# Kernel tuning notes

Measured on AMD Instinct MI355X. Metric: run time of the kernel, lower is better.

## Reference

```python
import jax, jax.numpy as jnp
import numpy as np

K = 3
DILATION = 1
DG = 1  # deformable groups


def _deform_conv2d(x, offsets, mask, weight, bias, k=K, dilation=DILATION, dg=DG):
    # x: [B, C, H, W]; offsets: [B, dg*2*k*k, H, W]; mask: [B, dg*k*k, H, W]
    # weight: [O, C, k, k]; bias: [O]
    B, C, H, W = x.shape
    O = weight.shape[0]
    Cg = C // dg
    kk = k * k
    pad = (k // 2) * dilation

    # base sampling grid per kernel tap (stride=1)
    ky, kx = jnp.meshgrid(jnp.arange(k), jnp.arange(k), indexing='ij')
    ky = ky.reshape(kk)
    kx = kx.reshape(kk)
    base_y = (jnp.arange(H)[None, :, None] - pad + ky[:, None, None] * dilation)  # [kk,H,1]
    base_x = (jnp.arange(W)[None, None, :] - pad + kx[:, None, None] * dilation)  # [kk,1,W]

    off = offsets.reshape(B, dg, kk, 2, H, W)
    py = base_y[None, None].astype(x.dtype) + off[:, :, :, 0]  # [B,dg,kk,H,W]
    px = base_x[None, None].astype(x.dtype) + off[:, :, :, 1]  # [B,dg,kk,H,W]

    y0 = jnp.floor(py)
    x0 = jnp.floor(px)
    wy1 = py - y0  # frac weights
    wx1 = px - x0
    wy0 = 1.0 - wy1
    wx0 = 1.0 - wx1

    img = x.reshape(B, dg, Cg, H * W)

    def gather(yi, xi):
        # yi, xi: float integer-valued coords [B,dg,kk,H,W]; zero outside bounds
        valid = (yi >= 0) & (yi <= H - 1) & (xi >= 0) & (xi <= W - 1)
        yc = jnp.clip(yi, 0, H - 1).astype(jnp.int32)
        xc = jnp.clip(xi, 0, W - 1).astype(jnp.int32)
        idx = (yc * W + xc).reshape(B, dg, 1, kk * H * W)
        vals = jnp.take_along_axis(img, idx, axis=3).reshape(B, dg, Cg, kk, H, W)
        return vals * valid.reshape(B, dg, 1, kk, H, W).astype(x.dtype)

    def w5(a):  # lift [B,dg,kk,H,W] -> [B,dg,1,kk,H,W]
        return a.reshape(B, dg, 1, kk, H, W)

    sampled = (gather(y0, x0) * w5(wy0 * wx0)
               + gather(y0, x0 + 1) * w5(wy0 * wx1)
               + gather(y0 + 1, x0) * w5(wy1 * wx0)
               + gather(y0 + 1, x0 + 1) * w5(wy1 * wx1))  # [B,dg,Cg,kk,H,W]

    sampled = sampled * mask.reshape(B, dg, 1, kk, H, W)
    sampled = sampled.reshape(B, C, kk, H, W)

    out = jnp.einsum('bckhw,ock->bohw', sampled, weight.reshape(O, C, kk))
    return out + bias[None, :, None, None]


def setup_inputs() -> dict:
    key = jax.random.key(0)
    k1, k2, k3, k4, k5 = jax.random.split(key, 5)
    B, C, O, H, W = 8, 128, 128, 64, 64
    x = jax.random.normal(k1, (B, C, H, W), dtype=jnp.float32)
    offsets = jax.random.normal(k2, (B, DG * 2 * K * K, H, W), dtype=jnp.float32)
    mask = jax.random.uniform(k3, (B, DG * K * K, H, W), dtype=jnp.float32)
    fan_in = C * K * K
    weight = jax.random.normal(k4, (O, C, K, K), dtype=jnp.float32) / np.sqrt(fan_in)
    bias = jax.random.normal(k5, (O,), dtype=jnp.float32) * 0.01
    return {"x": x, "offsets": offsets, "mask": mask, "weight": weight, "bias": bias}


def reference(x, offsets, mask, weight, bias):
    return _deform_conv2d(x, offsets, mask, weight, bias)
```

## Files before the change

### kernel.cpp

```cpp
#include <hip/hip_runtime.h>
#include <math.h>

constexpr int Bn = 8, Cn = 128, On = 128, Hn = 64, Wn = 64;
constexpr int KK = 9, PAD = 1, BDIM = 256;
constexpr int CG = 16;
constexpr int NG = Cn / CG;
constexpr int KG = 160;
constexpr int KTOT = NG * KG;
constexpr int BANDH = 10;
constexpr int XST = 656;
constexpr int AST = 168;
constexpr int ME = KK * Wn;

typedef __attribute__((ext_vector_type(8))) short bf16x8;
typedef __attribute__((ext_vector_type(4))) float f32x4;
typedef unsigned short u16;
typedef unsigned int u32;

__device__ inline u16 f2bf(float f) {
    union { float f; u32 u; } v; v.f = f;
    return (u16)((v.u + 0x7FFFu + ((v.u >> 16) & 1u)) >> 16);
}

__global__ void wprep_kernel(const float* __restrict__ w, u16* __restrict__ wbf) {
    const int e = blockIdx.x * BDIM + threadIdx.x;
    const int o  = e / KTOT;
    const int kp = e - o * KTOT;
    const int g  = kp / KG;
    const int r  = kp - g * KG;
    const int t  = r >> 4;
    const int cl = r & 15;
    float v = 0.f;
    if (t < KK) v = w[o * (Cn * KK) + (g * CG + cl) * KK + t];
    wbf[e] = f2bf(v);
}

__global__ __launch_bounds__(BDIM, 2)
void dcn_mfma_kernel(const float* __restrict__ x,
                     const float* __restrict__ offs,
                     const float* __restrict__ mask,
                     const u16*   __restrict__ wbf,
                     const float* __restrict__ bias,
                     float* __restrict__ out)
{
    __shared__ float xband[CG * XST];
    __shared__ u16   ash[Wn * AST];

    const int tid = threadIdx.x;
    const int b   = blockIdx.x & 7;
    const int h   = blockIdx.x >> 3;
    const int r0  = min(max(h - 4, 0), Hn - BANDH);

    const int cl16 = tid >> 4, l16b = tid & 15;
    float4 bnd[BANDH];
    {
        const float* xp = x + (((size_t)(b * Cn + cl16)) << 12) + r0 * Wn + (l16b << 2);
        #pragma unroll
        for (int r = 0; r < BANDH; ++r) bnd[r] = *(const float4*)(xp + r * Wn);
    }

    float4 mw[3]; int2 mq[3]; int2 mi[3];
    #pragma unroll
    for (int it = 0; it < 3; ++it) {
        mw[it] = make_float4(0.f, 0.f, 0.f, 0.f);
        mq[it] = make_int2(r0 << 8, r0 << 8);
        mi[it] = make_int2(7, 7);
        const int e = tid + it * BDIM;
        if (e < ME) {
            const int t = e >> 6, px = e & 63;
            const int ty = t / 3, tx = t - ty * 3;
            const float oy = offs[((b * 18 + 2 * t    ) * Hn + h) * Wn + px];
            const float ox = offs[((b * 18 + 2 * t + 1) * Hn + h) * Wn + px];
            const float m  = mask[((b * KK + t) * Hn + h) * Wn + px];
            const float py = (float)(h - PAD + ty) + oy;
            const float qx = (float)(px - PAD + tx) + ox;
            const float fy = floorf(py), fx = floorf(qx);
            const float wy1 = py - fy, wx1 = qx - fx;
            const float wy0 = 1.f - wy1, wx0 = 1.f - wx1;
            const int y0 = (int)fy, x0 = (int)fx;
            const bool cx0 = (x0 >= 0) && (x0 < Wn);
            const bool cx1 = (x0 >= -1) && (x0 < Wn - 1);
            const float wr[2] = { wy0, wy1 };
            float wout[4]; int qout[2], iout[2];
            #pragma unroll
            for (int j = 0; j < 2; ++j) {
                const int yr = y0 + j;
                const bool rv = (yr >= 0) && (yr < Hn);
                wout[2 * j]     = (rv && cx0) ? wr[j] * wx0 * m : 0.f;
                wout[2 * j + 1] = (rv && cx1) ? wr[j] * wx1 * m : 0.f;
                int qv;
                if (!rv || (!cx0 && !cx1)) qv = r0 << 8;
                else                       qv = (yr << 8) | (x0 + 1);
                const bool inband = (qv >> 8) >= r0 && (qv >> 8) < r0 + BANDH;
                qout[j] = inband ? qv : ~qv;
                iout[j] = (((qv >> 8) - r0) << 6) + (qv & 255) + 7;
            }
            mw[it] = make_float4(wout[0], wout[1], wout[2], wout[3]);
            mq[it] = make_int2(qout[0], qout[1]);
            mi[it] = make_int2(iout[0], iout[1]);
        }
    }

    {
        float* dp = &xband[cl16 * XST + 8 + (l16b << 2)];
        #pragma unroll
        for (int r = 0; r < BANDH; ++r) *(float4*)(dp + r * 64) = bnd[r];
        const int padi = (l16b < 8) ? l16b : (640 + l16b);
        xband[cl16 * XST + padi] = 0.f;
        const int px = tid & 63, kz = 144 + ((tid >> 6) << 2);
        u16* d = &ash[px * AST + kz];
        d[0] = 0; d[1] = 0; d[2] = 0; d[3] = 0;
    }
    __syncthreads();

    const int wv = tid >> 6, ln = tid & 63, quad = ln >> 4, l16 = ln & 15;
    const u16* wrow0 = wbf + (size_t)(wv * 32 + l16) * KTOT;

    f32x4 acc[2][4];
    #pragma unroll
    for (int mt = 0; mt < 2; ++mt)
        #pragma unroll
        for (int nt = 0; nt < 4; ++nt) acc[mt][nt] = (f32x4){0.f, 0.f, 0.f, 0.f};

    for (int g = 0; g < NG; ++g) {
        #pragma unroll
        for (int it = 0; it < 3; ++it) {
            const int e = tid + it * BDIM;
            if (e < ME) {
                const int t = e >> 6, px = e & 63;
                const float4 w  = mw[it];
                const int2   q  = mq[it];
                const int2   ix = mi[it];
                u16 av[CG];
                if (!__any((q.x | q.y) < 0)) {
                    #pragma unroll
                    for (int cl = 0; cl < CG; ++cl) {
                        const float* xc = &xband[cl * XST];
                        const float t0 = xc[ix.x], t1 = xc[ix.x + 1];
                        const float b0 = xc[ix.y], b1 = xc[ix.y + 1];
                        av[cl] = f2bf(fmaf(w.x, t0, fmaf(w.y, t1,
                                      fmaf(w.z, b0, w.w * b1))));
                    }
                } else {
                    const int qx = q.x < 0 ? ~q.x : q.x;
                    const int qy = q.y < 0 ? ~q.y : q.y;
                    const int yrx = qx >> 8, yry = qy >> 8;
                    const int xx = (qx & 255) - 1, xy = (qy & 255) - 1;
                    const int ax0 = max(xx, 0), ax1 = min(xx + 1, Wn - 1);
                    const int ay0 = max(xy, 0), ay1 = min(xy + 1, Wn - 1);
                    const float* gp = x + (((size_t)(b * Cn + g * CG)) << 12);
                    for (int cl = 0; cl < CG; ++cl) {
                        const float* gc = gp + (cl << 12);
                        const float t0 = gc[yrx * Wn + ax0], t1 = gc[yrx * Wn + ax1];
                        const float b0 = gc[yry * Wn + ay0], b1 = gc[yry * Wn + ay1];
                        av[cl] = f2bf(fmaf(w.x, t0, fmaf(w.y, t1,
                                      fmaf(w.z, b0, w.w * b1))));
                    }
                }
                u32 pk[8];
                #pragma unroll
                for (int q2 = 0; q2 < 8; ++q2)
                    pk[q2] = (u32)av[2 * q2] | ((u32)av[2 * q2 + 1] << 16);
                u32* d = (u32*)&ash[px * AST + (t << 4)];
                *(uint4*)d       = make_uint4(pk[0], pk[1], pk[2], pk[3]);
                *(uint4*)(d + 4) = make_uint4(pk[4], pk[5], pk[6], pk[7]);
            }
        }
        __syncthreads();

        if (g + 1 < NG) {
            const float* xp = x + (((size_t)(b * Cn + (g + 1) * CG + cl16)) << 12)
                              + r0 * Wn + (l16b << 2);
            #pragma unroll
            for (int r = 0; r < BANDH; ++r) bnd[r] = *(const float4*)(xp + r * Wn);
        }

        #pragma unroll
        for (int s = 0; s < 5; ++s) {
            const int kg = g * KG + s * 32 + quad * 8;
            const int kl = s * 32 + quad * 8;
            const bf16x8 a0 = *(const bf16x8*)(wrow0 + kg);
            const bf16x8 a1 = *(const bf16x8*)(wrow0 + 16 * KTOT + kg);
            const bf16x8 b0 = *(const bf16x8*)&ash[(0 * 16 + l16) * AST + kl];
            const bf16x8 b1 = *(const bf16x8*)&ash[(1 * 16 + l16) * AST + kl];
            const bf16x8 b2 = *(const bf16x8*)&ash[(2 * 16 + l16) * AST + kl];
            const bf16x8 b3 = *(const bf16x8*)&ash[(3 * 16 + l16) * AST + kl];
            acc[0][0] = __builtin_amdgcn_mfma_f32_16x16x32_bf16(a0, b0, acc[0][0], 0, 0, 0);
            acc[0][1] = __builtin_amdgcn_mfma_f32_16x16x32_bf16(a0, b1, acc[0][1], 0, 0, 0);
            acc[0][2] = __builtin_amdgcn_mfma_f32_16x16x32_bf16(a0, b2, acc[0][2], 0, 0, 0);
            acc[0][3] = __builtin_amdgcn_mfma_f32_16x16x32_bf16(a0, b3, acc[0][3], 0, 0, 0);
            acc[1][0] = __builtin_amdgcn_mfma_f32_16x16x32_bf16(a1, b0, acc[1][0], 0, 0, 0);
            acc[1][1] = __builtin_amdgcn_mfma_f32_16x16x32_bf16(a1, b1, acc[1][1], 0, 0, 0);
            acc[1][2] = __builtin_amdgcn_mfma_f32_16x16x32_bf16(a1, b2, acc[1][2], 0, 0, 0);
            acc[1][3] = __builtin_amdgcn_mfma_f32_16x16x32_bf16(a1, b3, acc[1][3], 0, 0, 0);
        }

        if (g + 1 < NG) {
            float* dp = &xband[cl16 * XST + 8 + (l16b << 2)];
            #pragma unroll
            for (int r = 0; r < BANDH; ++r) *(float4*)(dp + r * 64) = bnd[r];
        }
        __syncthreads();
    }

    float* ob = out + (((size_t)b * On) * Hn + h) * Wn;
    #pragma unroll
    for (int mt = 0; mt < 2; ++mt)
        #pragma unroll
        for (int nt = 0; nt < 4; ++nt)
            #pragma unroll
            for (int r = 0; r < 4; ++r) {
                const int o  = wv * 32 + mt * 16 + quad * 4 + r;
                const int px = nt * 16 + l16;
                ob[(size_t)o * (Hn * Wn) + px] = acc[mt][nt][r] + bias[o];
            }
}

constexpr int FB_PXB = 32, FB_CCH = 4, FB_NCT = FB_CCH * KK, FB_MW = KK * FB_PXB;

#define FMA4(A, S, W)                          \
    A.x = fmaf((S).x, (W), A.x);               \
    A.y = fmaf((S).y, (W), A.y);               \
    A.z = fmaf((S).z, (W), A.z);               \
    A.w = fmaf((S).w, (W), A.w);

__global__ __launch_bounds__(BDIM, 4)
void dcn_fb_kernel(const float* __restrict__ x,
                   const float* __restrict__ offs,
                   const float* __restrict__ mask,
                   const float* __restrict__ weight,
                   const float* __restrict__ bias,
                   float* __restrict__ out)
{
    __shared__ float wmeta[4 * FB_MW];
    __shared__ int   imeta[4 * FB_MW];
    __shared__ float ssh[FB_NCT * FB_PXB];
    __shared__ float wsh[FB_NCT * On];

    const int tid    = threadIdx.x;
    const int b      = blockIdx.x & 7;
    const int rem    = blockIdx.x >> 3;
    const int h      = rem >> 1;
    const int pxbase = (rem & 1) * FB_PXB;

    for (int e = tid; e < FB_MW; e += BDIM) {
        const int t  = e >> 5;
        const int px = e & 31;
        const int pg = pxbase + px;
        const int ty = t / 3, tx = t - ty * 3;
        const float oy = offs[((b * 18 + 2 * t    ) * Hn + h) * Wn + pg];
        const float ox = offs[((b * 18 + 2 * t + 1) * Hn + h) * Wn + pg];
        const float m  = mask[((b * KK + t) * Hn + h) * Wn + pg];
        const float py = (float)(h - PAD + ty) + oy;
        const float qx = (float)(pg - PAD + tx) + ox;
        const float y0 = floorf(py), x0 = floorf(qx);
        const float wy1 = py - y0, wx1 = qx - x0;
        const float wy0 = 1.f - wy1, wx0 = 1.f - wx1;
        const float cw[4] = { wy0 * wx0, wy0 * wx1, wy1 * wx0, wy1 * wx1 };
        #pragma unroll
        for (int k = 0; k < 4; ++k) {
            const float yk = y0 + (float)(k >> 1);
            const float xk = x0 + (float)(k & 1);
            const bool valid = (yk >= 0.f) && (yk <= (float)(Hn - 1)) &&
                               (xk >= 0.f) && (xk <= (float)(Wn - 1));
            const int yc = (int)fminf(fmaxf(yk, 0.f), (float)(Hn - 1));
            const int xc = (int)fminf(fmaxf(xk, 0.f), (float)(Wn - 1));
            wmeta[k * FB_MW + e] = valid ? cw[k] * m : 0.f;
            imeta[k * FB_MW + e] = yc * Wn + xc;
        }
    }
    __syncthreads();

    const int px0 = (tid & 7) << 2;
    const int oo  = (tid >> 3) << 2;

    float4 acc[4];
    #pragma unroll
    for (int j = 0; j < 4; ++j) acc[j] = make_float4(0.f, 0.f, 0.f, 0.f);

    for (int cb = 0; cb < Cn / FB_CCH; ++cb) {
        #pragma unroll
        for (int it = 0; it < (FB_NCT * On) / BDIM; ++it) {
            const int e = tid + it * BDIM;
            const int r = e >> 7;
            const int o = e & 127;
            wsh[r * On + o] = weight[o * (Cn * KK) + cb * FB_NCT + r];
        }
        for (int e = tid; e < FB_NCT * FB_PXB; e += BDIM) {
            const int px = e & 31;
            const int ct = e >> 5;
            const int c  = ct / 9;
            const int mb = (ct - c * 9) * FB_PXB + px;
            const float* xp = x + (((b * Cn) + cb * FB_CCH + c) << 12);
            float v =  wmeta[mb]              * xp[imeta[mb]];
            v = fmaf(wmeta[FB_MW     + mb], xp[imeta[FB_MW     + mb]], v);
            v = fmaf(wmeta[2 * FB_MW + mb], xp[imeta[2 * FB_MW + mb]], v);
            v = fmaf(wmeta[3 * FB_MW + mb], xp[imeta[3 * FB_MW + mb]], v);
            ssh[ct * FB_PXB + px] = v;
        }
        __syncthreads();

        #pragma unroll 6
        for (int ct = 0; ct < FB_NCT; ++ct) {
            const float4 sv = *(const float4*)&ssh[ct * FB_PXB + px0];
            const float4 wa = *(const float4*)&wsh[ct * On + oo];
            FMA4(acc[0], sv, wa.x);
            FMA4(acc[1], sv, wa.y);
            FMA4(acc[2], sv, wa.z);
            FMA4(acc[3], sv, wa.w);
        }
        __syncthreads();
    }

    #pragma unroll
    for (int j = 0; j < 4; ++j) {
        const float bv = bias[oo + j];
        float4 r = acc[j];
        r.x += bv; r.y += bv; r.z += bv; r.w += bv;
        *(float4*)&out[((b * On + oo + j) * Hn + h) * Wn + pxbase + px0] = r;
    }
}

extern "C" void kernel_launch(void* const* d_in, const int* in_sizes, int n_in,
                              void* d_out, int out_size, void* d_ws, size_t ws_size,
                              hipStream_t stream) {
    const float* x      = (const float*)d_in[0];
    const float* offs   = (const float*)d_in[1];
    const float* mask   = (const float*)d_in[2];
    const float* weight = (const float*)d_in[3];
    const float* bias   = (const float*)d_in[4];
    float* out = (float*)d_out;

    const size_t need = (size_t)On * KTOT * sizeof(u16);
    if (d_ws != nullptr && ws_size >= need) {
        u16* wbf = (u16*)d_ws;
        wprep_kernel<<<dim3(On * KTOT / BDIM), dim3(BDIM), 0, stream>>>(weight, wbf);
        dcn_mfma_kernel<<<dim3(Bn * Hn), dim3(BDIM), 0, stream>>>(
            x, offs, mask, wbf, bias, out);
    } else {
        dcn_fb_kernel<<<dim3(Bn * Hn * 2), dim3(BDIM), 0, stream>>>(
            x, offs, mask, weight, bias, out);
    }
}
```

Baseline: 157.5 us.

## Split MFMA deform-conv blocks into half-row tiles with bf16 channel-pair band

Each block now handles 32 output pixels instead of 64, doubling the grid and raising launch bounds to 4 blocks per CU to improve occupancy. The input band is stored in shared memory as bf16 channel pairs, which halves LDS footprint and the number of LDS reads per bilinear sample. Shared-memory strides are padded to odd word counts to avoid bank conflicts. Output is staged through LDS for coalesced float4 stores. The trade-off is extra rounding of the input to bf16 before interpolation, and the weight rows are reloaded by twice as many blocks.

```diff
diff --git a/kernel.cpp b/kernel.cpp
--- a/kernel.cpp
+++ b/kernel.cpp
@@ -3,14 +3,15 @@
 
 constexpr int Bn = 8, Cn = 128, On = 128, Hn = 64, Wn = 64;
 constexpr int KK = 9, PAD = 1, BDIM = 256;
+constexpr int PXB = 32;
 constexpr int CG = 16;
 constexpr int NG = Cn / CG;
 constexpr int KG = 160;
 constexpr int KTOT = NG * KG;
 constexpr int BANDH = 10;
-constexpr int XST = 656;
-constexpr int AST = 168;
-constexpr int ME = KK * Wn;
+constexpr int XSTP = 657;
+constexpr int AST = 170;
+constexpr int ME = KK * PXB;
 
 typedef __attribute__((ext_vector_type(8))) short bf16x8;
 typedef __attribute__((ext_vector_type(4))) float f32x4;
@@ -21,6 +22,11 @@
     union { float f; u32 u; } v; v.f = f;
     return (u16)((v.u + 0x7FFFu + ((v.u >> 16) & 1u)) >> 16);
 }
+__device__ inline u32 pk2bf(float a, float b) {
+    return (u32)f2bf(a) | ((u32)f2bf(b) << 16);
+}
+__device__ inline float bflo(u32 w) { return __uint_as_float(w << 16); }
+__device__ inline float bfhi(u32 w) { return __uint_as_float(w & 0xFFFF0000u); }
 
 __global__ void wprep_kernel(const float* __restrict__ w, u16* __restrict__ wbf) {
     const int e = blockIdx.x * BDIM + threadIdx.x;
@@ -35,7 +41,7 @@
     wbf[e] = f2bf(v);
 }
 
-__global__ __launch_bounds__(BDIM, 2)
+__global__ __launch_bounds__(BDIM, 4)
 void dcn_mfma_kernel(const float* __restrict__ x,
                      const float* __restrict__ offs,
                      const float* __restrict__ mask,
@@ -43,37 +49,45 @@
                      const float* __restrict__ bias,
                      float* __restrict__ out)
 {
-    __shared__ float xband[CG * XST];
-    __shared__ u16   ash[Wn * AST];
-
-    const int tid = threadIdx.x;
-    const int b   = blockIdx.x & 7;
-    const int h   = blockIdx.x >> 3;
-    const int r0  = min(max(h - 4, 0), Hn - BANDH);
-
-    const int cl16 = tid >> 4, l16b = tid & 15;
-    float4 bnd[BANDH];
+    __shared__ __align__(16) u32 pband[8 * XSTP];
+    __shared__ __align__(16) u16 ash[PXB * AST];
+
+    const int tid    = threadIdx.x;
+    const int b      = blockIdx.x & 7;
+    const int rem    = blockIdx.x >> 3;
+    const int h      = rem >> 1;
+    const int pxbase = (rem & 1) * PXB;
+    const int r0     = min(max(h - 4, 0), Hn - BANDH);
+
+    const int s_px4  = tid & 15;
+    const int s_pair = (tid >> 4) & 7;
+    float4 bnda[5], bndb[5];
     {
-        const float* xp = x + (((size_t)(b * Cn + cl16)) << 12) + r0 * Wn + (l16b << 2);
-        #pragma unroll
-        for (int r = 0; r < BANDH; ++r) bnd[r] = *(const float4*)(xp + r * Wn);
-    }
-
-    float4 mw[3]; int2 mq[3]; int2 mi[3];
-    #pragma unroll
-    for (int it = 0; it < 3; ++it) {
+        #pragma unroll
+        for (int it = 0; it < 5; ++it) {
+            const int row = (tid + it * BDIM) >> 7;
+            const float* base = x + (((size_t)(b * Cn + 2 * s_pair)) << 12)
+                                + (r0 + row) * Wn + (s_px4 << 2);
+            bnda[it] = *(const float4*)base;
+            bndb[it] = *(const float4*)(base + 4096);
+        }
+    }
+
+    float4 mw[2]; int2 mq[2]; int2 mi[2];
+    #pragma unroll
+    for (int it = 0; it < 2; ++it) {
         mw[it] = make_float4(0.f, 0.f, 0.f, 0.f);
         mq[it] = make_int2(r0 << 8, r0 << 8);
         mi[it] = make_int2(7, 7);
         const int e = tid + it * BDIM;
         if (e < ME) {
-            const int t = e >> 6, px = e & 63;
+            const int t = e >> 5, px = e & 31, pg = pxbase + px;
             const int ty = t / 3, tx = t - ty * 3;
-            const float oy = offs[((b * 18 + 2 * t    ) * Hn + h) * Wn + px];
-            const float ox = offs[((b * 18 + 2 * t + 1) * Hn + h) * Wn + px];
-            const float m  = mask[((b * KK + t) * Hn + h) * Wn + px];
+            const float oy = offs[((b * 18 + 2 * t    ) * Hn + h) * Wn + pg];
+            const float ox = offs[((b * 18 + 2 * t + 1) * Hn + h) * Wn + pg];
+            const float m  = mask[((b * KK + t) * Hn + h) * Wn + pg];
             const float py = (float)(h - PAD + ty) + oy;
-            const float qx = (float)(px - PAD + tx) + ox;
+            const float qx = (float)(pg - PAD + tx) + ox;
             const float fy = floorf(py), fx = floorf(qx);
             const float wy1 = py - fy, wx1 = qx - fx;
             const float wy0 = 1.f - wy1, wx0 = 1.f - wx1;
@@ -102,44 +116,53 @@
     }
 
     {
-        float* dp = &xband[cl16 * XST + 8 + (l16b << 2)];
-        #pragma unroll
-        for (int r = 0; r < BANDH; ++r) *(float4*)(dp + r * 64) = bnd[r];
-        const int padi = (l16b < 8) ? l16b : (640 + l16b);
-        xband[cl16 * XST + padi] = 0.f;
-        const int px = tid & 63, kz = 144 + ((tid >> 6) << 2);
-        u16* d = &ash[px * AST + kz];
-        d[0] = 0; d[1] = 0; d[2] = 0; d[3] = 0;
+        #pragma unroll
+        for (int it = 0; it < 5; ++it) {
+            const int row = (tid + it * BDIM) >> 7;
+            u32* d = &pband[s_pair * XSTP + row * 64 + 8 + (s_px4 << 2)];
+            d[0] = pk2bf(bnda[it].x, bndb[it].x);
+            d[1] = pk2bf(bnda[it].y, bndb[it].y);
+            d[2] = pk2bf(bnda[it].z, bndb[it].z);
+            d[3] = pk2bf(bnda[it].w, bndb[it].w);
+        }
+        if (tid < 128) {
+            const int pr = tid >> 4, ws = tid & 15;
+            pband[pr * XSTP + (ws < 8 ? ws : 640 + ws)] = 0;
+        }
+        ((u32*)ash)[(tid >> 3) * 85 + 72 + (tid & 7)] = 0;
     }
     __syncthreads();
 
     const int wv = tid >> 6, ln = tid & 63, quad = ln >> 4, l16 = ln & 15;
     const u16* wrow0 = wbf + (size_t)(wv * 32 + l16) * KTOT;
 
-    f32x4 acc[2][4];
+    f32x4 acc[2][2];
     #pragma unroll
     for (int mt = 0; mt < 2; ++mt)
         #pragma unroll
-        for (int nt = 0; nt < 4; ++nt) acc[mt][nt] = (f32x4){0.f, 0.f, 0.f, 0.f};
+        for (int nt = 0; nt < 2; ++nt) acc[mt][nt] = (f32x4){0.f, 0.f, 0.f, 0.f};
 
     for (int g = 0; g < NG; ++g) {
         #pragma unroll
-        for (int it = 0; it < 3; ++it) {
+        for (int it = 0; it < 2; ++it) {
             const int e = tid + it * BDIM;
             if (e < ME) {
-                const int t = e >> 6, px = e & 63;
+                const int t = e >> 5, px = e & 31;
                 const float4 w  = mw[it];
                 const int2   q  = mq[it];
                 const int2   ix = mi[it];
-                u16 av[CG];
+                u32 avp[8];
                 if (!__any((q.x | q.y) < 0)) {
                     #pragma unroll
-                    for (int cl = 0; cl < CG; ++cl) {
-                        const float* xc = &xband[cl * XST];
-                        const float t0 = xc[ix.x], t1 = xc[ix.x + 1];
-                        const float b0 = xc[ix.y], b1 = xc[ix.y + 1];
-                        av[cl] = f2bf(fmaf(w.x, t0, fmaf(w.y, t1,
-                                      fmaf(w.z, b0, w.w * b1))));
+                    for (int c2 = 0; c2 < 8; ++c2) {
+                        const u32* pc = &pband[c2 * XSTP];
+                        const u32 wt0 = pc[ix.x], wt1 = pc[ix.x + 1];
+                        const u32 wb0 = pc[ix.y], wb1 = pc[ix.y + 1];
+                        const float va = fmaf(w.x, bflo(wt0), fmaf(w.y, bflo(wt1),
+                                         fmaf(w.z, bflo(wb0), w.w * bflo(wb1))));
+                        const float vb = fmaf(w.x, bfhi(wt0), fmaf(w.y, bfhi(wt1),
+                                         fmaf(w.z, bfhi(wb0), w.w * bfhi(wb1))));
+                        avp[c2] = pk2bf(va, vb);
                     }
                 } else {
                     const int qx = q.x < 0 ? ~q.x : q.x;
@@ -149,71 +172,91 @@
                     const int ax0 = max(xx, 0), ax1 = min(xx + 1, Wn - 1);
                     const int ay0 = max(xy, 0), ay1 = min(xy + 1, Wn - 1);
                     const float* gp = x + (((size_t)(b * Cn + g * CG)) << 12);
-                    for (int cl = 0; cl < CG; ++cl) {
-                        const float* gc = gp + (cl << 12);
-                        const float t0 = gc[yrx * Wn + ax0], t1 = gc[yrx * Wn + ax1];
-                        const float b0 = gc[yry * Wn + ay0], b1 = gc[yry * Wn + ay1];
-                        av[cl] = f2bf(fmaf(w.x, t0, fmaf(w.y, t1,
-                                      fmaf(w.z, b0, w.w * b1))));
+                    for (int c2 = 0; c2 < 8; ++c2) {
+                        float v2[2];
+                        for (int sb = 0; sb < 2; ++sb) {
+                            const float* gc = gp + ((2 * c2 + sb) << 12);
+                            const float t0 = gc[yrx * Wn + ax0], t1 = gc[yrx * Wn + ax1];
+                            const float b0 = gc[yry * Wn + ay0], b1 = gc[yry * Wn + ay1];
+                            v2[sb] = fmaf(w.x, t0, fmaf(w.y, t1,
+                                     fmaf(w.z, b0, w.w * b1)));
+                        }
+                        avp[c2] = pk2bf(v2[0], v2[1]);
                     }
                 }
-                u32 pk[8];
+                u32* d = (u32*)ash + px * 85 + t * 8;
                 #pragma unroll
-                for (int q2 = 0; q2 < 8; ++q2)
-                    pk[q2] = (u32)av[2 * q2] | ((u32)av[2 * q2 + 1] << 16);
-                u32* d = (u32*)&ash[px * AST + (t << 4)];
-                *(uint4*)d       = make_uint4(pk[0], pk[1], pk[2], pk[3]);
-                *(uint4*)(d + 4) = make_uint4(pk[4], pk[5], pk[6], pk[7]);
+                for (int j = 0; j < 8; ++j) d[j] = avp[j];
             }
         }
         __syncthreads();
 
         if (g + 1 < NG) {
-            const float* xp = x + (((size_t)(b * Cn + (g + 1) * CG + cl16)) << 12)
-                              + r0 * Wn + (l16b << 2);
-            #pragma unroll
-            for (int r = 0; r < BANDH; ++r) bnd[r] = *(const float4*)(xp + r * Wn);
-        }
-
+            #pragma unroll
+            for (int it = 0; it < 5; ++it) {
+                const int row = (tid + it * BDIM) >> 7;
+                const float* base = x + (((size_t)(b * Cn + (g + 1) * CG + 2 * s_pair)) << 12)
+                                    + (r0 + row) * Wn + (s_px4 << 2);
+                bnda[it] = *(const float4*)base;
+                bndb[it] = *(const float4*)(base + 4096);
+            }
+        }
+
+        const u32* ad = (const u32*)ash;
         #pragma unroll
         for (int s = 0; s < 5; ++s) {
             const int kg = g * KG + s * 32 + quad * 8;
-            const int kl = s * 32 + quad * 8;
             const bf16x8 a0 = *(const bf16x8*)(wrow0 + kg);
             const bf16x8 a1 = *(const bf16x8*)(wrow0 + 16 * KTOT + kg);
-            const bf16x8 b0 = *(const bf16x8*)&ash[(0 * 16 + l16) * AST + kl];
-            const bf16x8 b1 = *(const bf16x8*)&ash[(1 * 16 + l16) * AST + kl];
-            const bf16x8 b2 = *(const bf16x8*)&ash[(2 * 16 + l16) * AST + kl];
-            const bf16x8 b3 = *(const bf16x8*)&ash[(3 * 16 + l16) * AST + kl];
-            acc[0][0] = __builtin_amdgcn_mfma_f32_16x16x32_bf16(a0, b0, acc[0][0], 0, 0, 0);
-            acc[0][1] = __builtin_amdgcn_mfma_f32_16x16x32_bf16(a0, b1, acc[0][1], 0, 0, 0);
-            acc[0][2] = __builtin_amdgcn_mfma_f32_16x16x32_bf16(a0, b2, acc[0][2], 0, 0, 0);
-            acc[0][3] = __builtin_amdgcn_mfma_f32_16x16x32_bf16(a0, b3, acc[0][3], 0, 0, 0);
-            acc[1][0] = __builtin_amdgcn_mfma_f32_16x16x32_bf16(a1, b0, acc[1][0], 0, 0, 0);
-            acc[1][1] = __builtin_amdgcn_mfma_f32_16x16x32_bf16(a1, b1, acc[1][1], 0, 0, 0);
-            acc[1][2] = __builtin_amdgcn_mfma_f32_16x16x32_bf16(a1, b2, acc[1][2], 0, 0, 0);
-            acc[1][3] = __builtin_amdgcn_mfma_f32_16x16x32_bf16(a1, b3, acc[1][3], 0, 0, 0);
+            union BF { bf16x8 v; u32 w[4]; } b0, b1;
+            const int kd = s * 16 + quad * 4;
+            #pragma unroll
+            for (int j = 0; j < 4; ++j) {
+                b0.w[j] = ad[(0 * 16 + l16) * 85 + kd + j];
+                b1.w[j] = ad[(1 * 16 + l16) * 85 + kd + j];
+            }
+            acc[0][0] = __builtin_amdgcn_mfma_f32_16x16x32_bf16(a0, b0.v, acc[0][0], 0, 0, 0);
+            acc[0][1] = __builtin_amdgcn_mfma_f32_16x16x32_bf16(a0, b1.v, acc[0][1], 0, 0, 0);
+            acc[1][0] = __builtin_amdgcn_mfma_f32_16x16x32_bf16(a1, b0.v, acc[1][0], 0, 0, 0);
+            acc[1][1] = __builtin_amdgcn_mfma_f32_16x16x32_bf16(a1, b1.v, acc[1][1], 0, 0, 0);
         }
 
         if (g + 1 < NG) {
-            float* dp = &xband[cl16 * XST + 8 + (l16b << 2)];
-            #pragma unroll
-            for (int r = 0; r < BANDH; ++r) *(float4*)(dp + r * 64) = bnd[r];
+            #pragma unroll
+            for (int it = 0; it < 5; ++it) {
+                const int row = (tid + it * BDIM) >> 7;
+                u32* d = &pband[s_pair * XSTP + row * 64 + 8 + (s_px4 << 2)];
+                d[0] = pk2bf(bnda[it].x, bndb[it].x);
+                d[1] = pk2bf(bnda[it].y, bndb[it].y);
+                d[2] = pk2bf(bnda[it].z, bndb[it].z);
+                d[3] = pk2bf(bnda[it].w, bndb[it].w);
+            }
         }
         __syncthreads();
     }
 
-    float* ob = out + (((size_t)b * On) * Hn + h) * Wn;
+    float* tr = (float*)pband;
     #pragma unroll
     for (int mt = 0; mt < 2; ++mt)
         #pragma unroll
-        for (int nt = 0; nt < 4; ++nt)
+        for (int nt = 0; nt < 2; ++nt)
             #pragma unroll
             for (int r = 0; r < 4; ++r) {
                 const int o  = wv * 32 + mt * 16 + quad * 4 + r;
                 const int px = nt * 16 + l16;
-                ob[(size_t)o * (Hn * Wn) + px] = acc[mt][nt][r] + bias[o];
-            }
+                tr[o * 36 + px] = acc[mt][nt][r] + bias[o];
+            }
+    __syncthreads();
+    float* ob = out + (size_t)b * On * Hn * Wn + h * Wn + pxbase;
+    {
+        const int orow = tid >> 3, ck = tid & 7;
+        #pragma unroll
+        for (int it = 0; it < 4; ++it) {
+            const int o = it * 32 + orow;
+            const float4 v = *(const float4*)&tr[o * 36 + (ck << 2)];
+            *(float4*)&ob[(size_t)o * (Hn * Wn) + (ck << 2)] = v;
+        }
+    }
 }
 
 constexpr int FB_PXB = 32, FB_CCH = 4, FB_NCT = FB_CCH * KK, FB_MW = KK * FB_PXB;
@@ -335,7 +378,7 @@
     if (d_ws != nullptr && ws_size >= need) {
         u16* wbf = (u16*)d_ws;
         wprep_kernel<<<dim3(On * KTOT / BDIM), dim3(BDIM), 0, stream>>>(weight, wbf);
-        dcn_mfma_kernel<<<dim3(Bn * Hn), dim3(BDIM), 0, stream>>>(
+        dcn_mfma_kernel<<<dim3(Bn * Hn * 2), dim3(BDIM), 0, stream>>>(
             x, offs, mask, wbf, bias, out);
     } else {
         dcn_fb_kernel<<<dim3(Bn * Hn * 2), dim3(BDIM), 0, stream>>>(
```

New measurement: 149.5 us. -5.1%, faster.
